# Optimization experiments

Hardware: AMD Instinct MI355X
Metric: run time of the kernel (lower is better)

The kernel has to match this reference:

```python
import jax, jax.numpy as jnp
import numpy as np

B, S, E, H = 2, 2048, 1024, 16
DH = E // H
SCALE = 1.0 / float(np.sqrt(E))  # note: original scales by 1/sqrt(hidden_dim), not head_dim


def _icl_mask(s):
    # triu(diagonal=0) is masked (-inf): only strictly-past positions visible,
    # except (0,0) which is explicitly unmasked so row 0 attends to itself.
    m = jnp.triu(jnp.ones((s, s), dtype=bool), k=0)
    return m.at[0, 0].set(False)


def setup_inputs() -> dict:
    key = jax.random.key(0)
    ks = jax.random.split(key, 7)
    mk = lambda k, shp: jax.random.normal(k, shp, dtype=jnp.float32)
    return {
        "q": mk(ks[0], (B, S, E)),
        "k": mk(ks[1], (B, S, E)),
        "v": mk(ks[2], (B, S, E)),
        "Wq": mk(ks[3], (E, E)) * 0.02,
        "Wk": mk(ks[4], (E, E)) * 0.02,
        "Wv": mk(ks[5], (E, E)) * 0.02,
        "Wo": mk(ks[6], (E, E)) * 0.02,
    }


def reference(q, k, v, Wq, Wk, Wv, Wo):
    b, s, e = q.shape
    h, dh = H, e // H
    # projections (nn.Linear: x @ W.T), split heads -> [b, h, s, dh]
    qh = (q @ Wq.T).reshape(b, s, h, dh).transpose(0, 2, 1, 3)
    kh = (k @ Wk.T).reshape(b, s, h, dh).transpose(0, 2, 1, 3)
    vh = (v @ Wv.T).reshape(b, s, h, dh).transpose(0, 2, 1, 3)
    scores = jnp.einsum("bhsd,bhtd->bhst", qh, kh) * SCALE  # [b,h,s,s]
    scores = jnp.where(_icl_mask(s), -jnp.inf, scores)
    probs = jax.nn.softmax(scores, axis=-1)
    out = jnp.einsum("bhst,bhtd->bhsd", probs, vh)
    out = out.transpose(0, 2, 1, 3).reshape(b, s, e)
    return out @ Wo.T
```

## Files before the change

kernel.cpp:

```cpp
#include <hip/hip_runtime.h>
#include <hip/hip_bf16.h>

typedef unsigned short u16;
typedef unsigned int u32;
typedef __bf16 bf16x8 __attribute__((ext_vector_type(8)));
typedef float float4_ __attribute__((ext_vector_type(4)));

#define B_ 2
#define S_ 2048
#define E_ 1024
#define H_ 16
#define DH_ 64
#define M_ (B_*S_)
#define E2_ (E_*E_)
#define SCALE_ 0.03125f
#define LOG2E_ 1.4426950408889634f

__device__ __forceinline__ u16 f2bf(float f) {
    unsigned int x = __float_as_uint(f);
    x += 0x7fffu + ((x >> 16) & 1u);
    return (u16)(x >> 16);
}

template <typename T> struct raw8;
template <> struct raw8<float> { float4_ lo, hi; };
template <> struct raw8<u16>   { bf16x8 v; };

__device__ __forceinline__ raw8<float> ldr8(const float* p) {
    raw8<float> r; const float4_* q = (const float4_*)p; r.lo = q[0]; r.hi = q[1]; return r;
}
__device__ __forceinline__ raw8<u16> ldr8(const u16* p) {
    raw8<u16> r; r.v = *(const bf16x8*)p; return r;
}
__device__ __forceinline__ bf16x8 cvt8(const raw8<u16>& r) { return r.v; }
__device__ __forceinline__ bf16x8 cvt8(const raw8<float>& r) {
    union { bf16x8 v; __hip_bfloat162 h[4]; } u;
    u.h[0] = __float22bfloat162_rn(float2{r.lo[0], r.lo[1]});
    u.h[1] = __float22bfloat162_rn(float2{r.lo[2], r.lo[3]});
    u.h[2] = __float22bfloat162_rn(float2{r.hi[0], r.hi[1]});
    u.h[3] = __float22bfloat162_rn(float2{r.hi[2], r.hi[3]});
    return u.v;
}
__device__ __forceinline__ bf16x8 ld8(const u16* p) { return *(const bf16x8*)p; }

__device__ __forceinline__ void async16(u16* lds, const u16* g) {
    __builtin_amdgcn_global_load_lds(
        (const __attribute__((address_space(1))) u32*)g,
        (__attribute__((address_space(3))) u32*)lds, 16, 0, 0);
}

__device__ __forceinline__ int swz32(int row, int col) {
    return row * 32 + ((((col >> 3) ^ (row & 3)) << 3) | (col & 7));
}

__global__ __launch_bounds__(256)
void conv_all_kernel(const float* __restrict__ q, const float* __restrict__ k,
                     const float* __restrict__ v,
                     const float* __restrict__ Wq, const float* __restrict__ Wk,
                     const float* __restrict__ Wv, const float* __restrict__ Wo,
                     u16* __restrict__ Xq, u16* __restrict__ Xk, u16* __restrict__ Xv,
                     u16* __restrict__ Wqb, u16* __restrict__ Wkb,
                     u16* __restrict__ Wvb, u16* __restrict__ Wob) {
    const int bid = blockIdx.x;
    const float* src;
    u16* dst;
    size_t base;
    if (bid < 6144) {
        const int which = bid >> 11, off = bid & 2047;
        src = which == 0 ? q : which == 1 ? k : v;
        dst = which == 0 ? Xq : which == 1 ? Xk : Xv;
        base = (size_t)off * 2048;
    } else {
        const int wb = bid - 6144;
        const int which = wb >> 9, off = wb & 511;
        src = which == 0 ? Wq : which == 1 ? Wk : which == 2 ? Wv : Wo;
        dst = which == 0 ? Wqb : which == 1 ? Wkb : which == 2 ? Wvb : Wob;
        base = (size_t)off * 2048;
    }
    const size_t i = base + (size_t)threadIdx.x * 8;
    *(bf16x8*)&dst[i] = cvt8(ldr8(&src[i]));
}

__global__ __launch_bounds__(256)
void proj_kernel(const u16* __restrict__ Xq, const u16* __restrict__ Xk, const u16* __restrict__ Xv,
                 const u16* __restrict__ Wqb, const u16* __restrict__ Wkb, const u16* __restrict__ Wvb,
                 u16* __restrict__ Qh, u16* __restrict__ Kh, u16* __restrict__ Vt) {
    const int z = blockIdx.z;
    const u16* A   = (z == 0) ? Xq : (z == 1) ? Xk : Xv;
    const u16* Wb  = (z == 0) ? Wqb : (z == 1) ? Wkb : Wvb;
    u16* C         = (z == 0) ? Qh : (z == 1) ? Kh : Vt;
    const float cscale = (z == 0) ? SCALE_ : 1.0f;
    const int transV = (z == 2);
    const int bm = blockIdx.x * 128, bn = blockIdx.y * 128;

    __shared__ u16 As[3][128 * 32];
    __shared__ u16 Bs[3][128 * 32];

    const int tid  = threadIdx.x;
    const int lane = tid & 63;
    const int w    = tid >> 6;
    const int wr   = (w >> 1) * 64, wc = (w & 1) * 64;
    const int m16  = lane & 15, quad = lane >> 4, q4 = quad * 4;

    const int row0 = tid >> 2, ch = tid & 3;
    const int csw  = ((ch ^ (row0 & 3)) * 8);
    const u16* ag0 = &A[(size_t)(bm + row0) * 1024 + csw];
    const u16* ag1 = &A[(size_t)(bm + row0 + 64) * 1024 + csw];
    const u16* wg0 = &Wb[(size_t)(bn + row0) * 1024 + csw];
    const u16* wg1 = &Wb[(size_t)(bn + row0 + 64) * 1024 + csw];

    float4_ acc[4][4];
#pragma unroll
    for (int i = 0; i < 4; i++)
#pragma unroll
        for (int j = 0; j < 4; j++) acc[i][j] = (float4_){0.f, 0.f, 0.f, 0.f};

    u16* A0 = &As[0][0]; u16* A1 = &As[1][0]; u16* A2 = &As[2][0];
    u16* B0 = &Bs[0][0]; u16* B1 = &Bs[1][0]; u16* B2 = &Bs[2][0];

    auto stage = [&](u16* Ab, u16* Bb, int t) {
        const size_t ko = (size_t)t * 32;
        async16((u16*)((char*)Ab + (size_t)tid * 16), ag0 + ko);
        async16((u16*)((char*)Ab + (size_t)tid * 16 + 4096), ag1 + ko);
        async16((u16*)((char*)Bb + (size_t)tid * 16), wg0 + ko);
        async16((u16*)((char*)Bb + (size_t)tid * 16 + 4096), wg1 + ko);
    };

    stage(A0, B0, 0);
    stage(A1, B1, 1);
    asm volatile("s_waitcnt vmcnt(4)" ::: "memory");
    __builtin_amdgcn_s_barrier();
    __builtin_amdgcn_sched_barrier(0);

    for (int t = 0; t < 32; t++) {
        stage(A2, B2, (t + 2 < 32) ? (t + 2) : 31);
        __builtin_amdgcn_sched_barrier(0);

        bf16x8 af[4], bfr[4];
#pragma unroll
        for (int rt = 0; rt < 4; rt++)
            af[rt] = *(const bf16x8*)&A0[swz32(wr + rt * 16 + m16, quad * 8)];
#pragma unroll
        for (int ct = 0; ct < 4; ct++)
            bfr[ct] = *(const bf16x8*)&B0[swz32(wc + ct * 16 + m16, quad * 8)];
#pragma unroll
        for (int rt = 0; rt < 4; rt++)
#pragma unroll
            for (int ct = 0; ct < 4; ct++)
                acc[rt][ct] = __builtin_amdgcn_mfma_f32_16x16x32_bf16(af[rt], bfr[ct], acc[rt][ct], 0, 0, 0);

        asm volatile("s_waitcnt vmcnt(4)" ::: "memory");
        __builtin_amdgcn_s_barrier();
        __builtin_amdgcn_sched_barrier(0);

        u16* ta = A0; A0 = A1; A1 = A2; A2 = ta;
        u16* tb = B0; B0 = B1; B1 = B2; B2 = tb;
    }
    asm volatile("s_waitcnt vmcnt(0)" ::: "memory");

#pragma unroll
    for (int rt = 0; rt < 4; rt++)
#pragma unroll
        for (int ct = 0; ct < 4; ct++)
#pragma unroll
            for (int r = 0; r < 4; r++) {
                int row = bm + wr + rt * 16 + q4 + r;
                int col = bn + wc + ct * 16 + m16;
                u16 val = f2bf(acc[rt][ct][r] * cscale);
                if (!transV) {
                    C[(size_t)row * 1024 + col] = val;
                } else {
                    int bb = row >> 11, s = row & 2047;
                    C[((size_t)(bb * 1024 + col)) * 2048 + s] = val;
                }
            }
}

__global__ __launch_bounds__(256)
void out_kernel(const u16* __restrict__ AO, const u16* __restrict__ Wob, float* __restrict__ C) {
    const int bm = blockIdx.x * 128, bn = blockIdx.y * 64;

    __shared__ u16 As[3][128 * 32];
    __shared__ u16 Bs[3][64 * 32];

    const int tid  = threadIdx.x;
    const int lane = tid & 63;
    const int w    = tid >> 6;
    const int m16  = lane & 15, quad = lane >> 4, q4 = quad * 4;
    const int c1   = tid + 256;

    const int swc = (((tid & 3) ^ ((tid >> 2) & 3)) * 8);
    const u16* ag0 = &AO[(size_t)(bm + (tid >> 2)) * 1024 + swc];
    const u16* ag1 = &AO[(size_t)(bm + (c1 >> 2)) * 1024 + swc];
    const u16* bg  = &Wob[(size_t)(bn + (tid >> 2)) * 1024 + swc];

    float4_ acc[2][4];
#pragma unroll
    for (int i = 0; i < 2; i++)
#pragma unroll
        for (int j = 0; j < 4; j++) acc[i][j] = (float4_){0.f, 0.f, 0.f, 0.f};

    u16* A0 = &As[0][0]; u16* A1 = &As[1][0]; u16* A2 = &As[2][0];
    u16* B0 = &Bs[0][0]; u16* B1 = &Bs[1][0]; u16* B2 = &Bs[2][0];

    auto stage = [&](u16* Ab, u16* Bb, int t) {
        const size_t ko = (size_t)t * 32;
        async16((u16*)((char*)Ab + (size_t)tid * 16), ag0 + ko);
        async16((u16*)((char*)Ab + (size_t)c1 * 16), ag1 + ko);
        async16((u16*)((char*)Bb + (size_t)tid * 16), bg + ko);
    };

    stage(A0, B0, 0);
    stage(A1, B1, 1);
    asm volatile("s_waitcnt vmcnt(3)" ::: "memory");
    __builtin_amdgcn_s_barrier();
    __builtin_amdgcn_sched_barrier(0);

    for (int t = 0; t < 32; t++) {
        stage(A2, B2, (t + 2 < 32) ? (t + 2) : 31);
        __builtin_amdgcn_sched_barrier(0);

        bf16x8 af[2], bfr[4];
#pragma unroll
        for (int rt = 0; rt < 2; rt++)
            af[rt] = *(const bf16x8*)&A0[swz32(w * 32 + rt * 16 + m16, quad * 8)];
#pragma unroll
        for (int ct = 0; ct < 4; ct++)
            bfr[ct] = *(const bf16x8*)&B0[swz32(ct * 16 + m16, quad * 8)];
#pragma unroll
        for (int rt = 0; rt < 2; rt++)
#pragma unroll
            for (int ct = 0; ct < 4; ct++)
                acc[rt][ct] = __builtin_amdgcn_mfma_f32_16x16x32_bf16(af[rt], bfr[ct], acc[rt][ct], 0, 0, 0);

        asm volatile("s_waitcnt vmcnt(3)" ::: "memory");
        __builtin_amdgcn_s_barrier();
        __builtin_amdgcn_sched_barrier(0);

        u16* ta = A0; A0 = A1; A1 = A2; A2 = ta;
        u16* tb = B0; B0 = B1; B1 = B2; B2 = tb;
    }
    asm volatile("s_waitcnt vmcnt(0)" ::: "memory");

#pragma unroll
    for (int rt = 0; rt < 2; rt++)
#pragma unroll
        for (int ct = 0; ct < 4; ct++)
#pragma unroll
            for (int r = 0; r < 4; r++) {
                int row = bm + w * 32 + rt * 16 + q4 + r;
                int col = bn + ct * 16 + m16;
                C[(size_t)row * 1024 + col] = acc[rt][ct][r];
            }
}

__device__ __forceinline__ int sw64(int row, int col) {
    return row * 64 + ((((col >> 3) ^ (row & 7)) << 3) | (col & 7));
}

__global__ __launch_bounds__(256, 2)
void attn_kernel(const u16* __restrict__ Qh, const u16* __restrict__ Kh,
                 const u16* __restrict__ Vt, u16* __restrict__ O) {
    const int h    = blockIdx.x;
    const int tq   = 31 - blockIdx.y;
    const int b    = blockIdx.z;
    const int tid  = threadIdx.x;
    const int lane = tid & 63;
    const int w    = tid >> 6;
    const int m16  = lane & 15;
    const int quad = lane >> 4;
    const int q4   = quad * 4;

    __shared__ u16 Ks[3][64 * 64];
    __shared__ u16 Vs[3][64 * 64];
    __shared__ u16 Ps[64 * 64];

    const int srow0 = tid >> 3;
    const int ssw   = (((tid & 7) ^ (srow0 & 7)) * 8);

    const size_t kbase = ((size_t)(b * S_)) * E_ + h * DH_;
    const size_t vbase = ((size_t)(b * 1024 + h * DH_)) * 2048;
    const u16* kg0 = &Kh[kbase + (size_t)srow0 * E_ + ssw];
    const u16* kg1 = kg0 + (size_t)32 * E_;
    const u16* vg0 = &Vt[vbase + (size_t)srow0 * 2048 + ssw];
    const u16* vg1 = vg0 + (size_t)32 * 2048;

    bf16x8 qf[2];
    {
        const u16* qa = Qh + ((size_t)(b * S_ + tq * 64 + w * 16 + m16)) * E_ + h * DH_;
        qf[0] = ld8(qa + quad * 8);
        qf[1] = ld8(qa + 32 + quad * 8);
    }

    float l_part[4] = {0.f, 0.f, 0.f, 0.f};
    float4_ o_acc[4];
#pragma unroll
    for (int dt = 0; dt < 4; dt++) o_acc[dt] = (float4_){0.f, 0.f, 0.f, 0.f};

    u16* k0 = &Ks[0][0]; u16* k1 = &Ks[1][0]; u16* k2 = &Ks[2][0];
    u16* v0 = &Vs[0][0]; u16* v1 = &Vs[1][0]; u16* v2 = &Vs[2][0];

    auto stage_to = [&](u16* kb, u16* vb, int tile) {
        const size_t ko = (size_t)tile * 64 * E_;
        const int    vo = tile * 64;
        async16(kb + tid * 8, kg0 + ko);
        async16(kb + (tid + 256) * 8, kg1 + ko);
        async16(vb + tid * 8, vg0 + vo);
        async16(vb + (tid + 256) * 8, vg1 + vo);
    };

    stage_to(k0, v0, 0);
    stage_to(k1, v1, tq > 0 ? 1 : 0);
    asm volatile("s_waitcnt vmcnt(4)" ::: "memory");
    __builtin_amdgcn_s_barrier();
    __builtin_amdgcn_sched_barrier(0);

    for (int t = 0; t <= tq; t++) {
        stage_to(k2, v2, (t + 2 <= tq) ? (t + 2) : tq);
        __builtin_amdgcn_sched_barrier(0);

        float4_ sc[4];
#pragma unroll
        for (int ct = 0; ct < 4; ct++) sc[ct] = (float4_){0.f, 0.f, 0.f, 0.f};
#pragma unroll
        for (int ks = 0; ks < 2; ks++)
#pragma unroll
            for (int ct = 0; ct < 4; ct++) {
                bf16x8 kf = *(const bf16x8*)&k0[sw64(ct * 16 + m16, ks * 32 + quad * 8)];
                sc[ct] = __builtin_amdgcn_mfma_f32_16x16x32_bf16(qf[ks], kf, sc[ct], 0, 0, 0);
            }

#pragma unroll
        for (int ct = 0; ct < 4; ct++) {
            float pp[4];
            if (t != tq) {
#pragma unroll
                for (int r = 0; r < 4; r++) {
                    pp[r] = exp2f(sc[ct][r] * LOG2E_);
                    l_part[r] += pp[r];
                }
            } else {
#pragma unroll
                for (int r = 0; r < 4; r++) {
                    int i_loc = w * 16 + q4 + r;
                    int j_loc = ct * 16 + m16;
                    bool allow = (j_loc < i_loc) || (tq == 0 && i_loc == 0 && j_loc == 0);
                    pp[r] = allow ? exp2f(sc[ct][r] * LOG2E_) : 0.f;
                    l_part[r] += pp[r];
                }
            }
            union { __hip_bfloat162 h2; u16 s[2]; } u01, u23;
            u01.h2 = __float22bfloat162_rn(float2{pp[0], pp[1]});
            u23.h2 = __float22bfloat162_rn(float2{pp[2], pp[3]});
            Ps[sw64(w * 16 + q4 + 0, ct * 16 + m16)] = u01.s[0];
            Ps[sw64(w * 16 + q4 + 1, ct * 16 + m16)] = u01.s[1];
            Ps[sw64(w * 16 + q4 + 2, ct * 16 + m16)] = u23.s[0];
            Ps[sw64(w * 16 + q4 + 3, ct * 16 + m16)] = u23.s[1];
        }

#pragma unroll
        for (int ks = 0; ks < 2; ks++) {
            bf16x8 pf = *(const bf16x8*)&Ps[sw64(w * 16 + m16, ks * 32 + quad * 8)];
#pragma unroll
            for (int dt = 0; dt < 4; dt++) {
                bf16x8 vf = *(const bf16x8*)&v0[sw64(dt * 16 + m16, ks * 32 + quad * 8)];
                o_acc[dt] = __builtin_amdgcn_mfma_f32_16x16x32_bf16(pf, vf, o_acc[dt], 0, 0, 0);
            }
        }

        asm volatile("s_waitcnt vmcnt(4)" ::: "memory");
        __builtin_amdgcn_s_barrier();
        __builtin_amdgcn_sched_barrier(0);

        u16* tk = k0; k0 = k1; k1 = k2; k2 = tk;
        u16* tv = v0; v0 = v1; v1 = v2; v2 = tv;
    }
    asm volatile("s_waitcnt vmcnt(0)" ::: "memory");

    const size_t obase = ((size_t)(b * S_ + tq * 64)) * E_ + h * DH_;
#pragma unroll
    for (int r = 0; r < 4; r++) {
        float l = l_part[r];
#pragma unroll
        for (int msk = 1; msk <= 8; msk <<= 1) l += __shfl_xor(l, msk);
        float inv_l = 1.0f / l;
        int row = w * 16 + q4 + r;
#pragma unroll
        for (int dt = 0; dt < 4; dt++) {
            int col = dt * 16 + m16;
            O[obase + (size_t)row * E_ + col] = f2bf(o_acc[dt][r] * inv_l);
        }
    }
}

extern "C" void kernel_launch(void* const* d_in, const int* in_sizes, int n_in,
                              void* d_out, int out_size, void* d_ws, size_t ws_size,
                              hipStream_t stream) {
    const float* q  = (const float*)d_in[0];
    const float* k  = (const float*)d_in[1];
    const float* v  = (const float*)d_in[2];
    const float* Wq = (const float*)d_in[3];
    const float* Wk = (const float*)d_in[4];
    const float* Wv = (const float*)d_in[5];
    const float* Wo = (const float*)d_in[6];

    const size_t ME = (size_t)M_ * E_;
    u16* ws  = (u16*)d_ws;
    u16* Qh  = ws;
    u16* Kh  = ws + ME;
    u16* Vt  = ws + 2 * ME;
    u16* AO  = ws + 3 * ME;
    u16* Wqb = AO;
    u16* Wkb = AO + E2_;
    u16* Wvb = AO + 2 * (size_t)E2_;
    u16* Wob = ws + 4 * ME;
    u16* Xv  = ws + 4 * ME + E2_;
    u16* Xq  = (u16*)d_out;
    u16* Xk  = Xq + ME;

    dim3 blk(256);
    conv_all_kernel<<<dim3(8192), blk, 0, stream>>>(q, k, v, Wq, Wk, Wv, Wo,
                                                    Xq, Xk, Xv, Wqb, Wkb, Wvb, Wob);
    proj_kernel<<<dim3(32, 8, 3), blk, 0, stream>>>(Xq, Xk, Xv, Wqb, Wkb, Wvb, Qh, Kh, Vt);
    attn_kernel<<<dim3(16, 32, 2), blk, 0, stream>>>(Qh, Kh, Vt, AO);
    out_kernel<<<dim3(32, 16), blk, 0, stream>>>(AO, Wob, (float*)d_out);
}
```

Measured before the change: 213.4 us.

## Fuse fp32-to-bf16 activation conversion into projection GEMM A-tile loads

Removes the separate conversion pass over q/k/v activations; the projection kernel now loads fp32 activations into registers, converts them to bf16 and writes them to swizzled LDS, prefetching two k-steps ahead. Only the weights are still converted in a standalone kernel. This removes a full write and re-read of the bf16 activation copies, but each proj block now reads fp32 (twice the bytes) and re-reads the activations for every N tile (8x). The A-operand path also loses the async global-to-LDS copy, which adds register pressure and VALU work inside the main loop.

```diff
diff --git a/kernel.cpp b/kernel.cpp
--- a/kernel.cpp
+++ b/kernel.cpp
@@ -54,39 +54,23 @@
 }
 
 __global__ __launch_bounds__(256)
-void conv_all_kernel(const float* __restrict__ q, const float* __restrict__ k,
-                     const float* __restrict__ v,
-                     const float* __restrict__ Wq, const float* __restrict__ Wk,
-                     const float* __restrict__ Wv, const float* __restrict__ Wo,
-                     u16* __restrict__ Xq, u16* __restrict__ Xk, u16* __restrict__ Xv,
-                     u16* __restrict__ Wqb, u16* __restrict__ Wkb,
-                     u16* __restrict__ Wvb, u16* __restrict__ Wob) {
-    const int bid = blockIdx.x;
-    const float* src;
-    u16* dst;
-    size_t base;
-    if (bid < 6144) {
-        const int which = bid >> 11, off = bid & 2047;
-        src = which == 0 ? q : which == 1 ? k : v;
-        dst = which == 0 ? Xq : which == 1 ? Xk : Xv;
-        base = (size_t)off * 2048;
-    } else {
-        const int wb = bid - 6144;
-        const int which = wb >> 9, off = wb & 511;
-        src = which == 0 ? Wq : which == 1 ? Wk : which == 2 ? Wv : Wo;
-        dst = which == 0 ? Wqb : which == 1 ? Wkb : which == 2 ? Wvb : Wob;
-        base = (size_t)off * 2048;
-    }
-    const size_t i = base + (size_t)threadIdx.x * 8;
-    *(bf16x8*)&dst[i] = cvt8(ldr8(&src[i]));
+void convw_kernel(const float* __restrict__ Wq, const float* __restrict__ Wk,
+                  const float* __restrict__ Wv, const float* __restrict__ Wo,
+                  u16* __restrict__ Wqb, u16* __restrict__ Wkb,
+                  u16* __restrict__ Wvb, u16* __restrict__ Wob) {
+    const int which = blockIdx.y;
+    const float* src = which == 0 ? Wq : which == 1 ? Wk : which == 2 ? Wv : Wo;
+    u16* dst        = which == 0 ? Wqb : which == 1 ? Wkb : which == 2 ? Wvb : Wob;
+    size_t off = ((size_t)blockIdx.x * 256 + threadIdx.x) * 8;
+    *(bf16x8*)&dst[off] = cvt8(ldr8(&src[off]));
 }
 
 __global__ __launch_bounds__(256)
-void proj_kernel(const u16* __restrict__ Xq, const u16* __restrict__ Xk, const u16* __restrict__ Xv,
+void proj_kernel(const float* __restrict__ q, const float* __restrict__ k, const float* __restrict__ v,
                  const u16* __restrict__ Wqb, const u16* __restrict__ Wkb, const u16* __restrict__ Wvb,
                  u16* __restrict__ Qh, u16* __restrict__ Kh, u16* __restrict__ Vt) {
     const int z = blockIdx.z;
-    const u16* A   = (z == 0) ? Xq : (z == 1) ? Xk : Xv;
+    const float* A = (z == 0) ? q : (z == 1) ? k : v;
     const u16* Wb  = (z == 0) ? Wqb : (z == 1) ? Wkb : Wvb;
     u16* C         = (z == 0) ? Qh : (z == 1) ? Kh : Vt;
     const float cscale = (z == 0) ? SCALE_ : 1.0f;
@@ -102,12 +86,12 @@
     const int wr   = (w >> 1) * 64, wc = (w & 1) * 64;
     const int m16  = lane & 15, quad = lane >> 4, q4 = quad * 4;
 
-    const int row0 = tid >> 2, ch = tid & 3;
+    const int row0 = tid >> 2, ch = tid & 3, row1 = row0 + 64;
     const int csw  = ((ch ^ (row0 & 3)) * 8);
-    const u16* ag0 = &A[(size_t)(bm + row0) * 1024 + csw];
-    const u16* ag1 = &A[(size_t)(bm + row0 + 64) * 1024 + csw];
+    const float* ag0 = &A[(size_t)(bm + row0) * 1024 + ch * 8];
+    const float* ag1 = &A[(size_t)(bm + row1) * 1024 + ch * 8];
     const u16* wg0 = &Wb[(size_t)(bn + row0) * 1024 + csw];
-    const u16* wg1 = &Wb[(size_t)(bn + row0 + 64) * 1024 + csw];
+    const u16* wg1 = &Wb[(size_t)(bn + row1) * 1024 + csw];
 
     float4_ acc[4][4];
 #pragma unroll
@@ -118,22 +102,34 @@
     u16* A0 = &As[0][0]; u16* A1 = &As[1][0]; u16* A2 = &As[2][0];
     u16* B0 = &Bs[0][0]; u16* B1 = &Bs[1][0]; u16* B2 = &Bs[2][0];
 
-    auto stage = [&](u16* Ab, u16* Bb, int t) {
+    const int wr0s = swz32(row0, ch * 8);
+    const int wr1s = swz32(row1, ch * 8);
+
+    auto stage_w = [&](u16* Bb, int t) {
         const size_t ko = (size_t)t * 32;
-        async16((u16*)((char*)Ab + (size_t)tid * 16), ag0 + ko);
-        async16((u16*)((char*)Ab + (size_t)tid * 16 + 4096), ag1 + ko);
         async16((u16*)((char*)Bb + (size_t)tid * 16), wg0 + ko);
         async16((u16*)((char*)Bb + (size_t)tid * 16 + 4096), wg1 + ko);
     };
 
-    stage(A0, B0, 0);
-    stage(A1, B1, 1);
-    asm volatile("s_waitcnt vmcnt(4)" ::: "memory");
+    raw8<float> pa0 = ldr8(ag0);
+    raw8<float> pa1 = ldr8(ag1);
+    *(bf16x8*)&A0[wr0s] = cvt8(pa0);
+    *(bf16x8*)&A0[wr1s] = cvt8(pa1);
+    stage_w(B0, 0);
+    stage_w(B1, 1);
+    pa0 = ldr8(ag0 + 32);
+    pa1 = ldr8(ag1 + 32);
+    asm volatile("s_waitcnt vmcnt(6) lgkmcnt(0)" ::: "memory");
     __builtin_amdgcn_s_barrier();
     __builtin_amdgcn_sched_barrier(0);
 
     for (int t = 0; t < 32; t++) {
-        stage(A2, B2, (t + 2 < 32) ? (t + 2) : 31);
+        *(bf16x8*)&A1[wr0s] = cvt8(pa0);
+        *(bf16x8*)&A1[wr1s] = cvt8(pa1);
+        const int tn = (t + 2 < 32) ? (t + 2) : 31;
+        pa0 = ldr8(ag0 + (size_t)tn * 32);
+        pa1 = ldr8(ag1 + (size_t)tn * 32);
+        stage_w(B2, tn);
         __builtin_amdgcn_sched_barrier(0);
 
         bf16x8 af[4], bfr[4];
@@ -149,7 +145,7 @@
             for (int ct = 0; ct < 4; ct++)
                 acc[rt][ct] = __builtin_amdgcn_mfma_f32_16x16x32_bf16(af[rt], bfr[ct], acc[rt][ct], 0, 0, 0);
 
-        asm volatile("s_waitcnt vmcnt(4)" ::: "memory");
+        asm volatile("s_waitcnt vmcnt(6) lgkmcnt(0)" ::: "memory");
         __builtin_amdgcn_s_barrier();
         __builtin_amdgcn_sched_barrier(0);
 
@@ -414,14 +410,10 @@
     u16* Wkb = AO + E2_;
     u16* Wvb = AO + 2 * (size_t)E2_;
     u16* Wob = ws + 4 * ME;
-    u16* Xv  = ws + 4 * ME + E2_;
-    u16* Xq  = (u16*)d_out;
-    u16* Xk  = Xq + ME;
 
     dim3 blk(256);
-    conv_all_kernel<<<dim3(8192), blk, 0, stream>>>(q, k, v, Wq, Wk, Wv, Wo,
-                                                    Xq, Xk, Xv, Wqb, Wkb, Wvb, Wob);
-    proj_kernel<<<dim3(32, 8, 3), blk, 0, stream>>>(Xq, Xk, Xv, Wqb, Wkb, Wvb, Qh, Kh, Vt);
+    convw_kernel<<<dim3(512, 4), blk, 0, stream>>>(Wq, Wk, Wv, Wo, Wqb, Wkb, Wvb, Wob);
+    proj_kernel<<<dim3(32, 8, 3), blk, 0, stream>>>(q, k, v, Wqb, Wkb, Wvb, Qh, Kh, Vt);
     attn_kernel<<<dim3(16, 32, 2), blk, 0, stream>>>(Qh, Kh, Vt, AO);
     out_kernel<<<dim3(32, 16), blk, 0, stream>>>(AO, Wob, (float*)d_out);
 }
```

New measurement: 214.6 us. Within noise of the previous version (+0.6%).
